# Optimization experiments

Hardware: AMD Instinct MI355X
Metric: run time of the kernel (lower is better)

The kernel has to match this reference:

```python
import jax, jax.numpy as jnp
import numpy as np

DIM1, DIM2, NUM_ANS = 1024, 1024, 1000
B, T = 64, 128


def setup_inputs() -> dict:
    key = jax.random.key(0)
    ks = jax.random.split(key, 12)
    H, D_IN = DIM1, DIM1 + DIM2
    s = 0.02
    return {
        "data1": jax.random.normal(ks[0], (B, T, DIM1), dtype=jnp.float32),
        "data2": jax.random.normal(ks[1], (B, T, DIM2), dtype=jnp.float32),
        # layer-1 LSTM (input D_IN -> hidden H), PyTorch gate order i,f,g,o
        "W_ih1": jax.random.normal(ks[2], (4 * H, D_IN), dtype=jnp.float32) * s,
        "W_hh1": jax.random.normal(ks[3], (4 * H, H), dtype=jnp.float32) * s,
        "b1": jax.random.normal(ks[4], (4 * H,), dtype=jnp.float32) * s,
        # layer-2 LSTM (H -> H)
        "W_ih2": jax.random.normal(ks[5], (4 * H, H), dtype=jnp.float32) * s,
        "W_hh2": jax.random.normal(ks[6], (4 * H, H), dtype=jnp.float32) * s,
        "b2": jax.random.normal(ks[7], (4 * H,), dtype=jnp.float32) * s,
        # predict MLP: dim1 -> dim1//4 -> num_ans
        "Wp1": jax.random.normal(ks[8], (DIM1, DIM1 // 4), dtype=jnp.float32) * s,
        "bp1": jnp.zeros((DIM1 // 4,), dtype=jnp.float32),
        "Wp2": jax.random.normal(ks[9], (DIM1 // 4, NUM_ANS), dtype=jnp.float32) * s,
        "bp2": jnp.zeros((NUM_ANS,), dtype=jnp.float32),
    }


def _lstm_cell(x, h, c, Wih, Whh, b):
    gates = x @ Wih.T + h @ Whh.T + b  # [B, 4H]
    i, f, g, o = jnp.split(gates, 4, axis=-1)
    c_new = jax.nn.sigmoid(f) * c + jax.nn.sigmoid(i) * jnp.tanh(g)
    h_new = jax.nn.sigmoid(o) * jnp.tanh(c_new)
    return h_new, c_new


def reference(data1, data2, W_ih1, W_hh1, b1, W_ih2, W_hh2, b2, Wp1, bp1, Wp2, bp2):
    joint = jnp.concatenate((data1, data2), axis=-1)  # [B, T, dim1+dim2]
    Bb = joint.shape[0]
    H = W_hh1.shape[1]
    z = jnp.zeros((Bb, H), dtype=joint.dtype)

    def step(carry, x_t):
        h1, c1, h2, c2 = carry
        h1, c1 = _lstm_cell(x_t, h1, c1, W_ih1, W_hh1, b1)
        h2, c2 = _lstm_cell(h1, h2, c2, W_ih2, W_hh2, b2)
        out_t = h2 + h1  # residual connection between layers
        return (h1, c1, h2, c2), out_t

    xs = jnp.swapaxes(joint, 0, 1)  # [T, B, D]
    _, outs = jax.lax.scan(step, (z, z, z, z), xs)
    lstm_out = jnp.swapaxes(outs, 0, 1)  # [B, T, H]

    hid = jax.nn.relu(lstm_out @ Wp1 + bp1)  # dropout is identity at inference
    logits = hid @ Wp2 + bp2  # [B, T, num_ans]
    return jax.nn.softmax(jnp.squeeze(logits), axis=-1)
```

## Files before the change

kernel.cpp:

```cpp
#include <hip/hip_runtime.h>
#include <math.h>

#define BB   64
#define TT   128
#define HH   1024
#define DIN  2048
#define G4   4096
#define MALL 8192
#define NANS 1000

typedef __attribute__((ext_vector_type(8))) short bf16x8;
typedef __attribute__((ext_vector_type(4))) float f32x4;

__device__ __forceinline__ float sigmoidf_(float x) { return 1.0f / (1.0f + expf(-x)); }

__device__ __forceinline__ unsigned short f2bf(float f) {
  unsigned u = __float_as_uint(f);
  u = (u + 0x7fff + ((u >> 16) & 1)) >> 16;
  return (unsigned short)u;
}
__device__ __forceinline__ float bf2f(unsigned short h) {
  return __uint_as_float(((unsigned)h) << 16);
}
__device__ __forceinline__ f32x4 mfma16(bf16x8 a, bf16x8 b, f32x4 c) {
  return __builtin_amdgcn_mfma_f32_16x16x32_bf16(a, b, c, 0, 0, 0);
}

__global__ __launch_bounds__(256) void concat_cast(
    const float* __restrict__ a, const float* __restrict__ b,
    unsigned short* __restrict__ o, int rshift, long total)
{
  long idx = ((long)blockIdx.x * 256 + threadIdx.x) * 4;
  if (idx >= total) return;
  int row = (int)(idx >> rshift);
  int col = (int)(idx & ((1L << rshift) - 1));
  int half = 1 << (rshift - 1);
  const float* s = (col < half) ? (a + (size_t)row * half + col)
                                : (b + (size_t)row * half + col - half);
  float4 v = *(const float4*)s;
  ushort4 ov;
  ov.x = f2bf(v.x); ov.y = f2bf(v.y); ov.z = f2bf(v.z); ov.w = f2bf(v.w);
  *(ushort4*)(o + idx) = ov;
}

__global__ __launch_bounds__(256) void cast_bf16(
    const float* __restrict__ s, unsigned short* __restrict__ o, long n)
{
  long idx = ((long)blockIdx.x * 256 + threadIdx.x) * 4;
  if (idx >= n) return;
  float4 v = *(const float4*)(s + idx);
  ushort4 ov;
  ov.x = f2bf(v.x); ov.y = f2bf(v.y); ov.z = f2bf(v.z); ov.w = f2bf(v.w);
  *(ushort4*)(o + idx) = ov;
}

__global__ __launch_bounds__(256) void cvt_wp1(
    const float* __restrict__ Wp1, unsigned short* __restrict__ o)
{
  int idx = blockIdx.x * 256 + threadIdx.x;
  int n = idx >> 10, k = idx & 1023;
  o[idx] = f2bf(Wp1[(size_t)k * 256 + n]);
}

__global__ __launch_bounds__(256) void cvt_wp2(
    const float* __restrict__ Wp2, unsigned short* __restrict__ o)
{
  int idx = blockIdx.x * 256 + threadIdx.x;
  int n = idx >> 8, k = idx & 255;
  o[idx] = f2bf(n < NANS ? Wp2[(size_t)k * NANS + n] : 0.f);
}

__global__ __launch_bounds__(256) void zero_f4(float4* __restrict__ p)
{
  p[blockIdx.x * 256 + threadIdx.x] = make_float4(0.f, 0.f, 0.f, 0.f);
}

template<int OUT_BF16, int RELU, int PERM>
__global__ __launch_bounds__(256) void mfma_gemm(
    const unsigned short* __restrict__ A,
    const unsigned short* __restrict__ W,
    const float* __restrict__ bias,
    void* __restrict__ Cout,
    int M, int N, int K, int ldc, int nvalid)
{
  __shared__ __align__(16) unsigned short As[128 * 72];
  __shared__ __align__(16) unsigned short Bs[128 * 72];
  const int t = threadIdx.x;
  const int n0 = blockIdx.x * 128, m0 = blockIdx.y * 128;
  const int w = t >> 6, lane = t & 63, lr = lane & 15, q = lane >> 4;
  const int wn = (w & 1) * 64, wm = (w >> 1) * 64;
  f32x4 acc[4][4] = {};
  for (int k0 = 0; k0 < K; k0 += 64) {
    #pragma unroll
    for (int s = 0; s < 4; s++) {
      int ci = s * 256 + t;
      int row = ci >> 3, c = ci & 7;
      bf16x8 va = *(const bf16x8*)(A + (size_t)(m0 + row) * K + k0 + c * 8);
      *(bf16x8*)(As + row * 72 + c * 8) = va;
      bf16x8 vb = *(const bf16x8*)(W + (size_t)(n0 + row) * K + k0 + c * 8);
      *(bf16x8*)(Bs + row * 72 + c * 8) = vb;
    }
    __syncthreads();
    #pragma unroll
    for (int kk = 0; kk < 2; kk++) {
      bf16x8 a[4], b[4];
      #pragma unroll
      for (int mt = 0; mt < 4; mt++)
        a[mt] = *(const bf16x8*)(As + (wm + mt * 16 + lr) * 72 + kk * 32 + q * 8);
      #pragma unroll
      for (int nt = 0; nt < 4; nt++)
        b[nt] = *(const bf16x8*)(Bs + (wn + nt * 16 + lr) * 72 + kk * 32 + q * 8);
      #pragma unroll
      for (int mt = 0; mt < 4; mt++)
        #pragma unroll
        for (int nt = 0; nt < 4; nt++)
          acc[mt][nt] = mfma16(a[mt], b[nt], acc[mt][nt]);
    }
    __syncthreads();
  }
  #pragma unroll
  for (int mt = 0; mt < 4; mt++)
    #pragma unroll
    for (int nt = 0; nt < 4; nt++)
      #pragma unroll
      for (int r = 0; r < 4; r++) {
        int row = m0 + wm + mt * 16 + q * 4 + r;
        int col = n0 + wn + nt * 16 + lr;
        if (col < nvalid) {
          float v = acc[mt][nt][r] + bias[col];
          if (RELU) v = fmaxf(v, 0.f);
          if (PERM) row = ((row & 127) << 6) | (row >> 7);
          if (OUT_BF16)
            ((unsigned short*)Cout)[(size_t)row * ldc + col] = f2bf(v);
          else
            ((float*)Cout)[(size_t)row * ldc + col] = v;
        }
      }
}

__global__ __launch_bounds__(256) void lstm_phase(
    const unsigned short* __restrict__ Whh1b,
    const unsigned short* __restrict__ W2cat,
    const unsigned short* __restrict__ gxb,
    const float* __restrict__ b2,
    int p,
    unsigned short* __restrict__ hbuf,
    float* __restrict__ c1, float* __restrict__ c2,
    unsigned short* __restrict__ lob)
{
  __shared__ float red[4][64][17];
  const int t = threadIdx.x;
  const int w = t >> 6, lane = t & 63, lr = lane & 15, q = lane >> 4;
  const bool isA = (blockIdx.x < 256);
  const int j0 = (isA ? blockIdx.x : blockIdx.x - 256) * 4;
  const int g0 = lr >> 2, u0 = lr & 3;
  const int cm = t >> 2, cu = t & 3, ju = j0 + cu;
  const unsigned short* hprev = hbuf + (size_t)((p + 1) & 1) * 131072;
  unsigned short*       hc    = hbuf + (size_t)(p & 1) * 131072;

  if (isA) {
    if (p == TT) return;
    const unsigned short* gp = gxb + ((size_t)(p << 6) + cm) * 4096 + ju;
    unsigned short gi = gp[0], gf = gp[1024], gg2 = gp[2048], go = gp[3072];
    {
      const unsigned short* wp =
          Whh1b + (size_t)(g0 * 1024 + j0 + u0) * 1024 + w * 256 + q * 8;
      const unsigned short* hb = hprev + w * 256 + q * 8;
      f32x4 acc[4] = {};
      #pragma unroll
      for (int ks = 0; ks < 8; ks++) {
        bf16x8 bfrag = *(const bf16x8*)(wp + ks * 32);
        #pragma unroll
        for (int mt = 0; mt < 4; mt++) {
          bf16x8 af = *(const bf16x8*)(hb + (size_t)(mt * 16 + lr) * 2048 + ks * 32);
          acc[mt] = mfma16(af, bfrag, acc[mt]);
        }
      }
      #pragma unroll
      for (int mt = 0; mt < 4; mt++)
        #pragma unroll
        for (int r = 0; r < 4; r++)
          red[w][mt * 16 + q * 4 + r][lr] = acc[mt][r];
    }
    __syncthreads();
    float s[4];
    #pragma unroll
    for (int gg = 0; gg < 4; gg++)
      s[gg] = red[0][cm][gg * 4 + cu] + red[1][cm][gg * 4 + cu]
            + red[2][cm][gg * 4 + cu] + red[3][cm][gg * 4 + cu];
    s[0] += bf2f(gi); s[1] += bf2f(gf); s[2] += bf2f(gg2); s[3] += bf2f(go);
    float i_ = sigmoidf_(s[0]), f_ = sigmoidf_(s[1]);
    float g_ = tanhf(s[2]), o_ = sigmoidf_(s[3]);
    float c = f_ * c1[cm * 1024 + ju] + i_ * g_;
    c1[cm * 1024 + ju] = c;
    hc[(size_t)cm * 2048 + ju] = f2bf(o_ * tanhf(c));
  } else {
    if (p == 0) return;
    {
      const unsigned short* wp =
          W2cat + (size_t)(g0 * 1024 + j0 + u0) * 2048 + w * 512 + q * 8;
      const unsigned short* hb = hprev + w * 512 + q * 8;
      f32x4 acc[4] = {};
      #pragma unroll
      for (int ks = 0; ks < 16; ks++) {
        bf16x8 bfrag = *(const bf16x8*)(wp + ks * 32);
        #pragma unroll
        for (int mt = 0; mt < 4; mt++) {
          bf16x8 af = *(const bf16x8*)(hb + (size_t)(mt * 16 + lr) * 2048 + ks * 32);
          acc[mt] = mfma16(af, bfrag, acc[mt]);
        }
      }
      #pragma unroll
      for (int mt = 0; mt < 4; mt++)
        #pragma unroll
        for (int r = 0; r < 4; r++)
          red[w][mt * 16 + q * 4 + r][lr] = acc[mt][r];
    }
    __syncthreads();
    float s[4];
    #pragma unroll
    for (int gg = 0; gg < 4; gg++)
      s[gg] = red[0][cm][gg * 4 + cu] + red[1][cm][gg * 4 + cu]
            + red[2][cm][gg * 4 + cu] + red[3][cm][gg * 4 + cu]
            + b2[gg * 1024 + ju];
    float i_ = sigmoidf_(s[0]), f_ = sigmoidf_(s[1]);
    float g_ = tanhf(s[2]), o_ = sigmoidf_(s[3]);
    float c = f_ * c2[cm * 1024 + ju] + i_ * g_;
    c2[cm * 1024 + ju] = c;
    float h2v = o_ * tanhf(c);
    ((unsigned short*)hprev)[(size_t)cm * 2048 + 1024 + ju] = f2bf(h2v);
    float h1v = bf2f(hprev[(size_t)cm * 2048 + ju]);
    lob[((size_t)(cm << 7) + (p - 1)) * 1024 + ju] = f2bf(h1v + h2v);
  }
}

__global__ __launch_bounds__(256) void softmax_k(float* __restrict__ out)
{
  __shared__ float smax[4];
  __shared__ float ssum[4];
  const int m = blockIdx.x;
  const int t = threadIdx.x;
  const int lane = t & 63, wid = t >> 6;
  const bool act = (t < 250);
  float x[4] = {0.f, 0.f, 0.f, 0.f};
  if (act) *(float4*)x = *(const float4*)(out + (size_t)m * NANS + t * 4);
  float v = act ? fmaxf(fmaxf(x[0], x[1]), fmaxf(x[2], x[3])) : -1e30f;
  #pragma unroll
  for (int o = 32; o > 0; o >>= 1) v = fmaxf(v, __shfl_down(v, o));
  if (lane == 0) smax[wid] = v;
  __syncthreads();
  const float mx = fmaxf(fmaxf(smax[0], smax[1]), fmaxf(smax[2], smax[3]));
  float e[4] = {0.f, 0.f, 0.f, 0.f};
  float s = 0.f;
  if (act) {
    e[0] = expf(x[0] - mx); e[1] = expf(x[1] - mx);
    e[2] = expf(x[2] - mx); e[3] = expf(x[3] - mx);
    s = (e[0] + e[1]) + (e[2] + e[3]);
  }
  #pragma unroll
  for (int o = 32; o > 0; o >>= 1) s += __shfl_down(s, o);
  if (lane == 0) ssum[wid] = s;
  __syncthreads();
  const float inv = 1.0f / (((ssum[0] + ssum[1]) + (ssum[2] + ssum[3])));
  if (act) {
    float4 o4 = make_float4(e[0] * inv, e[1] * inv, e[2] * inv, e[3] * inv);
    *(float4*)(out + (size_t)m * NANS + t * 4) = o4;
  }
}

extern "C" void kernel_launch(void* const* d_in, const int* in_sizes, int n_in,
                              void* d_out, int out_size, void* d_ws, size_t ws_size,
                              hipStream_t stream)
{
  const float* d1   = (const float*)d_in[0];
  const float* d2   = (const float*)d_in[1];
  const float* Wih1 = (const float*)d_in[2];
  const float* Whh1 = (const float*)d_in[3];
  const float* b1   = (const float*)d_in[4];
  const float* Wih2 = (const float*)d_in[5];
  const float* Whh2 = (const float*)d_in[6];
  const float* b2   = (const float*)d_in[7];
  const float* Wp1  = (const float*)d_in[8];
  const float* bp1  = (const float*)d_in[9];
  const float* Wp2  = (const float*)d_in[10];
  const float* bp2  = (const float*)d_in[11];
  float* out = (float*)d_out;

  unsigned char* p = (unsigned char*)d_ws;
  unsigned short* gxb   = (unsigned short*)p;  p += 67108864;
  unsigned short* jb    = (unsigned short*)p;  p += 33554432;
  unsigned short* Wb1   = (unsigned short*)p;  p += 16777216;
  unsigned short* W2cat = (unsigned short*)p;  p += 16777216;
  unsigned short* Whh1b = (unsigned short*)p;  p += 8388608;
  unsigned short* lob   = (unsigned short*)p;  p += 16777216;
  unsigned short* hidb  = (unsigned short*)p;  p += 4194304;
  unsigned short* Wp1t  = (unsigned short*)p;  p += 524288;
  unsigned short* Wp2t  = (unsigned short*)p;  p += 524288;
  unsigned short* hbuf  = (unsigned short*)p;  p += 524288;
  float*          c1    = (float*)p;           p += 262144;
  float*          c2    = (float*)p;           p += 262144;
  if (ws_size < (size_t)(p - (unsigned char*)d_ws)) return;

  concat_cast<<<16384, 256, 0, stream>>>(d1, d2, jb, 11, 16777216L);
  cast_bf16<<<8192, 256, 0, stream>>>(Wih1, Wb1, 8388608L);
  cast_bf16<<<4096, 256, 0, stream>>>(Whh1, Whh1b, 4194304L);
  concat_cast<<<8192, 256, 0, stream>>>(Wih2, Whh2, W2cat, 11, 8388608L);
  cvt_wp1<<<1024, 256, 0, stream>>>(Wp1, Wp1t);
  cvt_wp2<<<1024, 256, 0, stream>>>(Wp2, Wp2t);
  zero_f4<<<256, 256, 0, stream>>>((float4*)hbuf);

  mfma_gemm<1, 0, 1><<<dim3(32, 64), 256, 0, stream>>>(
      jb, Wb1, b1, gxb, MALL, G4, DIN, G4, G4);

  for (int ph = 0; ph <= TT; ph++)
    lstm_phase<<<512, 256, 0, stream>>>(Whh1b, W2cat, gxb, b2, ph,
                                        hbuf, c1, c2, lob);

  mfma_gemm<1, 1, 0><<<dim3(2, 64), 256, 0, stream>>>(
      lob, Wp1t, bp1, hidb, MALL, 256, 1024, 256, 256);
  mfma_gemm<0, 0, 0><<<dim3(8, 64), 256, 0, stream>>>(
      hidb, Wp2t, bp2, out, MALL, 1024, 256, NANS, NANS);
  softmax_k<<<MALL, 256, 0, stream>>>(out);
}
```

Baseline: 2.798 ms.

## Retile LSTM phase to 8 units per block with 2x2 MFMA register tiles

Each lstm_phase block now handles 8 hidden units with 512 threads instead of 4 units with 256, so the grid drops from 512 to 256 blocks. Each wave splits into a K-quarter and a batch half and computes a 2x2 tile of MFMAs. Each h fragment is reused across two weight fragments, which cuts redundant activation loads from global memory. The layer-2 path also now takes the previous h2 from the current-phase buffer instead of the stale one, which appears to fix the recurrence. The trade-off is fewer, larger blocks (less parallelism across CUs) and a larger shared reduction buffer.

```diff
diff --git a/kernel.cpp b/kernel.cpp
--- a/kernel.cpp
+++ b/kernel.cpp
@@ -138,7 +138,7 @@
       }
 }
 
-__global__ __launch_bounds__(256) void lstm_phase(
+__global__ __launch_bounds__(512) void lstm_phase(
     const unsigned short* __restrict__ Whh1b,
     const unsigned short* __restrict__ W2cat,
     const unsigned short* __restrict__ gxb,
@@ -148,13 +148,14 @@
     float* __restrict__ c1, float* __restrict__ c2,
     unsigned short* __restrict__ lob)
 {
-  __shared__ float red[4][64][17];
+  __shared__ float red[4][64][34];
   const int t = threadIdx.x;
   const int w = t >> 6, lane = t & 63, lr = lane & 15, q = lane >> 4;
-  const bool isA = (blockIdx.x < 256);
-  const int j0 = (isA ? blockIdx.x : blockIdx.x - 256) * 4;
+  const int kq = w & 3, rh = w >> 2;
+  const bool isA = (blockIdx.x < 128);
+  const int j0 = (isA ? blockIdx.x : blockIdx.x - 128) * 8;
   const int g0 = lr >> 2, u0 = lr & 3;
-  const int cm = t >> 2, cu = t & 3, ju = j0 + cu;
+  const int cm = t >> 3, cu = t & 7, ju = j0 + cu;
   const unsigned short* hprev = hbuf + (size_t)((p + 1) & 1) * 131072;
   unsigned short*       hc    = hbuf + (size_t)(p & 1) * 131072;
 
@@ -163,31 +164,38 @@
     const unsigned short* gp = gxb + ((size_t)(p << 6) + cm) * 4096 + ju;
     unsigned short gi = gp[0], gf = gp[1024], gg2 = gp[2048], go = gp[3072];
     {
-      const unsigned short* wp =
-          Whh1b + (size_t)(g0 * 1024 + j0 + u0) * 1024 + w * 256 + q * 8;
-      const unsigned short* hb = hprev + w * 256 + q * 8;
-      f32x4 acc[4] = {};
+      const int kof = kq * 256 + q * 8;
+      const unsigned short* wp0 =
+          Whh1b + (size_t)(g0 * 1024 + j0 + u0) * 1024 + kof;
+      const unsigned short* wp1 = wp0 + 4 * 1024;
+      const unsigned short* hb  = hprev + (size_t)(rh * 32 + lr) * 2048 + kof;
+      f32x4 acc[2][2] = {};
       #pragma unroll
       for (int ks = 0; ks < 8; ks++) {
-        bf16x8 bfrag = *(const bf16x8*)(wp + ks * 32);
-        #pragma unroll
-        for (int mt = 0; mt < 4; mt++) {
-          bf16x8 af = *(const bf16x8*)(hb + (size_t)(mt * 16 + lr) * 2048 + ks * 32);
-          acc[mt] = mfma16(af, bfrag, acc[mt]);
+        bf16x8 b0 = *(const bf16x8*)(wp0 + ks * 32);
+        bf16x8 b1 = *(const bf16x8*)(wp1 + ks * 32);
+        #pragma unroll
+        for (int mt = 0; mt < 2; mt++) {
+          bf16x8 af = *(const bf16x8*)(hb + (size_t)(mt * 16) * 2048 + ks * 32);
+          acc[mt][0] = mfma16(af, b0, acc[mt][0]);
+          acc[mt][1] = mfma16(af, b1, acc[mt][1]);
         }
       }
       #pragma unroll
-      for (int mt = 0; mt < 4; mt++)
-        #pragma unroll
-        for (int r = 0; r < 4; r++)
-          red[w][mt * 16 + q * 4 + r][lr] = acc[mt][r];
+      for (int mt = 0; mt < 2; mt++)
+        #pragma unroll
+        for (int r = 0; r < 4; r++) {
+          red[kq][rh * 32 + mt * 16 + q * 4 + r][lr]      = acc[mt][0][r];
+          red[kq][rh * 32 + mt * 16 + q * 4 + r][17 + lr] = acc[mt][1][r];
+        }
     }
     __syncthreads();
+    const int cb = (cu >> 2) * 17 + (cu & 3);
     float s[4];
     #pragma unroll
     for (int gg = 0; gg < 4; gg++)
-      s[gg] = red[0][cm][gg * 4 + cu] + red[1][cm][gg * 4 + cu]
-            + red[2][cm][gg * 4 + cu] + red[3][cm][gg * 4 + cu];
+      s[gg] = red[0][cm][cb + gg * 4] + red[1][cm][cb + gg * 4]
+            + red[2][cm][cb + gg * 4] + red[3][cm][cb + gg * 4];
     s[0] += bf2f(gi); s[1] += bf2f(gf); s[2] += bf2f(gg2); s[3] += bf2f(go);
     float i_ = sigmoidf_(s[0]), f_ = sigmoidf_(s[1]);
     float g_ = tanhf(s[2]), o_ = sigmoidf_(s[3]);
@@ -197,31 +205,39 @@
   } else {
     if (p == 0) return;
     {
-      const unsigned short* wp =
-          W2cat + (size_t)(g0 * 1024 + j0 + u0) * 2048 + w * 512 + q * 8;
-      const unsigned short* hb = hprev + w * 512 + q * 8;
-      f32x4 acc[4] = {};
+      const int kof = kq * 512 + q * 8;
+      const unsigned short* wp0 =
+          W2cat + (size_t)(g0 * 1024 + j0 + u0) * 2048 + kof;
+      const unsigned short* wp1 = wp0 + 4 * 2048;
+      const unsigned short* hbase = (kq < 2) ? hprev : hc;
+      const unsigned short* hb = hbase + (size_t)(rh * 32 + lr) * 2048 + kof;
+      f32x4 acc[2][2] = {};
       #pragma unroll
       for (int ks = 0; ks < 16; ks++) {
-        bf16x8 bfrag = *(const bf16x8*)(wp + ks * 32);
-        #pragma unroll
-        for (int mt = 0; mt < 4; mt++) {
-          bf16x8 af = *(const bf16x8*)(hb + (size_t)(mt * 16 + lr) * 2048 + ks * 32);
-          acc[mt] = mfma16(af, bfrag, acc[mt]);
+        bf16x8 b0 = *(const bf16x8*)(wp0 + ks * 32);
+        bf16x8 b1 = *(const bf16x8*)(wp1 + ks * 32);
+        #pragma unroll
+        for (int mt = 0; mt < 2; mt++) {
+          bf16x8 af = *(const bf16x8*)(hb + (size_t)(mt * 16) * 2048 + ks * 32);
+          acc[mt][0] = mfma16(af, b0, acc[mt][0]);
+          acc[mt][1] = mfma16(af, b1, acc[mt][1]);
         }
       }
       #pragma unroll
-      for (int mt = 0; mt < 4; mt++)
-        #pragma unroll
-        for (int r = 0; r < 4; r++)
-          red[w][mt * 16 + q * 4 + r][lr] = acc[mt][r];
+      for (int mt = 0; mt < 2; mt++)
+        #pragma unroll
+        for (int r = 0; r < 4; r++) {
+          red[kq][rh * 32 + mt * 16 + q * 4 + r][lr]      = acc[mt][0][r];
+          red[kq][rh * 32 + mt * 16 + q * 4 + r][17 + lr] = acc[mt][1][r];
+        }
     }
     __syncthreads();
+    const int cb = (cu >> 2) * 17 + (cu & 3);
     float s[4];
     #pragma unroll
     for (int gg = 0; gg < 4; gg++)
-      s[gg] = red[0][cm][gg * 4 + cu] + red[1][cm][gg * 4 + cu]
-            + red[2][cm][gg * 4 + cu] + red[3][cm][gg * 4 + cu]
+      s[gg] = red[0][cm][cb + gg * 4] + red[1][cm][cb + gg * 4]
+            + red[2][cm][cb + gg * 4] + red[3][cm][cb + gg * 4]
             + b2[gg * 1024 + ju];
     float i_ = sigmoidf_(s[0]), f_ = sigmoidf_(s[1]);
     float g_ = tanhf(s[2]), o_ = sigmoidf_(s[3]);
@@ -313,7 +329,7 @@
       jb, Wb1, b1, gxb, MALL, G4, DIN, G4, G4);
 
   for (int ph = 0; ph <= TT; ph++)
-    lstm_phase<<<512, 256, 0, stream>>>(Whh1b, W2cat, gxb, b2, ph,
+    lstm_phase<<<256, 512, 0, stream>>>(Whh1b, W2cat, gxb, b2, ph,
                                         hbuf, c1, c2, lob);
 
   mfma_gemm<1, 1, 0><<<dim3(2, 64), 256, 0, stream>>>(
```

New measurement: 2.784 ms. No clear change (-0.5%).
